# Kernel tuning notes

Hardware: AMD Instinct MI355X
Metric: run time of the kernel (lower is better)

The kernel has to match this reference:

```python
import jax, jax.numpy as jnp
import numpy as np

GROUPS = 4
ITER_N = 5


def conv1x1(x, w, b=None):
    # x: (B,C,N,W), w: (O,C)
    y = jnp.einsum('oc,bcnw->bonw', w, x)
    if b is not None:
        y = y + b[None, :, None, None]
    return y


def instance_norm(x, eps=1e-3):
    mu = x.mean(axis=(2, 3), keepdims=True)
    var = x.var(axis=(2, 3), keepdims=True)
    return (x - mu) * jax.lax.rsqrt(var + eps)


def batch_norm(x, g, b, eps=1e-5):
    mu = x.mean(axis=(0, 2, 3), keepdims=True)
    var = x.var(axis=(0, 2, 3), keepdims=True)
    return (x - mu) * jax.lax.rsqrt(var + eps) * g[None, :, None, None] + b[None, :, None, None]


def group_norm(x, g, b, groups=GROUPS, eps=1e-5):
    B, C, N, W = x.shape
    xg = x.reshape(B, groups, C // groups, N, W)
    mu = xg.mean(axis=(2, 3, 4), keepdims=True)
    var = xg.var(axis=(2, 3, 4), keepdims=True)
    xn = ((xg - mu) * jax.lax.rsqrt(var + eps)).reshape(B, C, N, W)
    return xn * g[None, :, None, None] + b[None, :, None, None]


def ns_sqrtm(A, iterN=ITER_N):
    # A: (..., d, d) SPD. MPNCOV Newton-Schulz matrix square root.
    d = A.shape[-1]
    I = jnp.eye(d, dtype=A.dtype)
    trA = jnp.trace(A, axis1=-2, axis2=-1)[..., None, None]
    An = A / trA
    ZY = 0.5 * (3.0 * I - An)
    Y = An @ ZY
    Z = ZY
    for _ in range(iterN - 2):  # fixed small loop over NS iterations
        ZY = 0.5 * (3.0 * I - Z @ Y)
        Y = Y @ ZY
        Z = ZY @ Z
    ZY = 0.5 * (Y @ (3.0 * I - Z @ Y))
    return ZY * jnp.sqrt(trA)


def covar_attn(feat):
    # feat: (B,C,N,W); per-group covariance pooling + sqrtm + channel reweight
    B, C, N, W = feat.shape
    d = C // GROUPS
    M = N * W
    f = feat.reshape(B, GROUPS, d, M)
    fc = f - f.mean(axis=-1, keepdims=True)
    cov = jnp.einsum('bgim,bgjm->bgij', fc, fc) / M  # == x I_hat x^T
    sq = ns_sqrtm(cov)
    s = sq.mean(axis=-2)  # torch.mean(cov_mat_sqrt, 1): mean over rows -> (B,G,d)
    return s.reshape(B, C, 1, 1) * feat


def setup_inputs() -> dict:
    key = jax.random.key(0)
    ks = jax.random.split(key, 4)
    B, C, N, W = 32, 128, 4000, 1
    scale = 1.0 / np.sqrt(C)
    return {
        'x': jax.random.normal(ks[0], (B, C, N, W), jnp.float32),
        'w_linear': jax.random.normal(ks[1], (C, C), jnp.float32) * scale,
        'gn_gamma': jnp.ones((C,), jnp.float32),
        'gn_beta': jnp.zeros((C,), jnp.float32),
        'bn1_g': jnp.ones((C,), jnp.float32),
        'bn1_b': jnp.zeros((C,), jnp.float32),
        'conv1_w': jax.random.normal(ks[2], (C, C), jnp.float32) * scale,
        'conv1_b': jnp.zeros((C,), jnp.float32),
        'bn2_g': jnp.ones((C,), jnp.float32),
        'bn2_b': jnp.zeros((C,), jnp.float32),
        'conv2_w': jax.random.normal(ks[3], (C, C), jnp.float32) * scale,
        'conv2_b': jnp.zeros((C,), jnp.float32),
    }


def reference(x, w_linear, gn_gamma, gn_beta, bn1_g, bn1_b, conv1_w, conv1_b, bn2_g, bn2_b, conv2_w, conv2_b):
    feat = conv1x1(x, w_linear)
    feat_attn = covar_attn(feat)
    y = group_norm(feat_attn + x, gn_gamma, gn_beta)
    # PointCN residual block (inchannel == outchannel -> identity shortcut)
    h = jax.nn.relu(batch_norm(instance_norm(y), bn1_g, bn1_b))
    h = conv1x1(h, conv1_w, conv1_b)
    h = jax.nn.relu(batch_norm(instance_norm(h), bn2_g, bn2_b))
    h = conv1x1(h, conv2_w, conv2_b)
    return h + y
```

## Files before the change

kernel.cpp:

```cpp
#include <hip/hip_runtime.h>

constexpr int Bn = 32;
constexpr int Cn = 128;
constexpr int Mn = 4000;
constexpr int Gn = 4;
constexpr int Dn = 32;
constexpr float GN_EPS = 1e-5f;
constexpr float IN_EPS = 1e-3f;
constexpr float BN_EPS = 1e-5f;

typedef __attribute__((ext_vector_type(8))) short bf16x8;
typedef __attribute__((ext_vector_type(4))) float f32x4;
typedef __attribute__((ext_vector_type(16))) float f32x16;

__device__ __forceinline__ float bf2f(ushort u) {
    union { unsigned int u; float f; } v;
    v.u = ((unsigned int)u) << 16;
    return v.f;
}
__device__ __forceinline__ ushort f2bf(float f) {
    union { float f; unsigned int u; } v;
    v.f = f;
    unsigned int r = v.u + 0x7FFFu + ((v.u >> 16) & 1u);
    return (ushort)(r >> 16);
}

__global__ void prep_w3(const float* __restrict__ w0, const float* __restrict__ w1,
                        const float* __restrict__ w2, ushort* __restrict__ wb,
                        float* __restrict__ zbase, int zquads) {
    const int i = blockIdx.x * 256 + threadIdx.x;
    const int which = i >> 14;
    const int off = i & 16383;
    const float v = (which == 0) ? w0[off] : (which == 1) ? w1[off] : w2[off];
    wb[i] = f2bf(v);
    if (i < zquads) {
        f32x4 z;
        z[0] = 0.f; z[1] = 0.f; z[2] = 0.f; z[3] = 0.f;
        *(f32x4*)(zbase + (size_t)i * 4) = z;
    }
}

__launch_bounds__(256)
__global__ void prep_xt(const float* __restrict__ x, ushort* __restrict__ xt) {
    __shared__ float tl[128 * 33];
    const int mb = blockIdx.x * 32, b = blockIdx.y;
    const int tid = threadIdx.x;
    const int mi = tid & 31, cg = tid >> 5;
#pragma unroll
    for (int p = 0; p < 16; ++p) {
        const int ci = cg + 8 * p;
        tl[ci * 33 + mi] = x[((size_t)b * Cn + ci) * Mn + mb + mi];
    }
    __syncthreads();
#pragma unroll
    for (int q = 0; q < 2; ++q) {
        const int row = (tid >> 4) + 16 * q;
        const int c8 = (tid & 15) * 8;
        bf16x8 v;
#pragma unroll
        for (int e = 0; e < 8; ++e)
            v[e] = (short)f2bf(tl[(c8 + e) * 33 + row]);
        *(bf16x8*)(xt + ((size_t)b * Mn + mb + row) * Cn + c8) = v;
    }
}

constexpr int WPAD = 136;
constexpr int EP0  = 132;

__launch_bounds__(256, 2)
__global__ void mgemm0_cov(const ushort* __restrict__ Wb,
                           const ushort* __restrict__ src,
                           ushort* __restrict__ dst_bf,
                           float* __restrict__ sf, float* __restrict__ sf2,
                           float* __restrict__ sfxp,
                           float* __restrict__ sxp, float* __restrict__ sx2p,
                           float* __restrict__ covp)
{
    __shared__ ushort Wl[128 * WPAD];
    __shared__ ushort El[64 * EP0];
    const int b = blockIdx.y;
    const int mb0 = blockIdx.x * 256;
    const int tid = threadIdx.x;
    const int wv = tid >> 6, l = tid & 63;
    const int li = l & 15, lg = l >> 4;

#pragma unroll
    for (int p = 0; p < 8; ++p) {
        const int u = tid + 256 * p;
        const int o = u >> 4, c8 = (u & 15) * 8;
        *(bf16x8*)&Wl[o * WPAD + c8] = *(const bf16x8*)(Wb + (size_t)o * 128 + c8);
    }
    __syncthreads();

    f32x16 cacc;
#pragma unroll
    for (int i = 0; i < 16; ++i) cacc[i] = 0.f;
    float s1a[8] = {}, s2a[8] = {}, s3a[8] = {}, s4a[8] = {}, s5a[8] = {};

    const int c8s = (tid & 15) * 8;
    const int cg = wv * 32 + (l & 31);
    const int kb8 = (l >> 5) * 8;

#pragma unroll 1
    for (int t = 0; t < 4; ++t) {
        const int mb = mb0 + t * 64;
        const int ma = mb + wv * 16 + li;
        const bool mok = ma < Mn;
        const size_t qrow = ((size_t)b * Mn + (mok ? ma : (Mn - 1))) * Cn;

        bf16x8 fr[4];
#pragma unroll
        for (int kb = 0; kb < 4; ++kb)
            fr[kb] = *(const bf16x8*)(src + qrow + kb * 32 + 8 * lg);

        f32x4 acc[8];
#pragma unroll
        for (int j = 0; j < 8; ++j)
#pragma unroll
            for (int r = 0; r < 4; ++r) acc[j][r] = 0.f;

#pragma unroll
        for (int kb = 0; kb < 4; ++kb) {
            const int cl = kb * 32 + 8 * lg;
#pragma unroll
            for (int j = 0; j < 8; ++j) {
                const bf16x8 bj = *(const bf16x8*)&Wl[(j * 16 + li) * WPAD + cl];
                acc[j] = __builtin_amdgcn_mfma_f32_16x16x32_bf16(fr[kb], bj, acc[j], 0, 0, 0);
            }
        }

        __syncthreads();
#pragma unroll
        for (int j = 0; j < 8; ++j) {
            const int o = j * 16 + li;
#pragma unroll
            for (int r = 0; r < 4; ++r) {
                const int ml = wv * 16 + lg * 4 + r;
                El[ml * EP0 + o] = (mb + ml < Mn) ? f2bf(acc[j][r]) : (ushort)0;
            }
        }
        __syncthreads();

#pragma unroll
        for (int p = 0; p < 4; ++p) {
            const int row = (tid >> 4) + 16 * p;
            const int m = mb + row;
            const bf16x8 v8 = *(const bf16x8*)&El[row * EP0 + c8s];
            if (m < Mn) {
                const size_t q = ((size_t)b * Mn + m) * Cn + c8s;
                *(bf16x8*)(dst_bf + q) = v8;
                const bf16x8 x8 = *(const bf16x8*)(src + q);
#pragma unroll
                for (int e = 0; e < 8; ++e) {
                    const float f = bf2f((ushort)v8[e]);
                    const float xv = bf2f((ushort)x8[e]);
                    s1a[e] += f;
                    s2a[e] = fmaf(f, f, s2a[e]);
                    s3a[e] = fmaf(f, xv, s3a[e]);
                    s4a[e] += xv;
                    s5a[e] = fmaf(xv, xv, s5a[e]);
                }
            }
        }

#pragma unroll
        for (int ks = 0; ks < 4; ++ks) {
            bf16x8 fgr;
#pragma unroll
            for (int e = 0; e < 8; ++e)
                fgr[e] = (short)El[(ks * 16 + kb8 + e) * EP0 + cg];
            cacc = __builtin_amdgcn_mfma_f32_32x32x16_bf16(fgr, fgr, cacc, 0, 0, 0);
        }
    }

    __syncthreads();
#pragma unroll
    for (int e = 0; e < 8; ++e) {
        s1a[e] += __shfl_xor(s1a[e], 16); s1a[e] += __shfl_xor(s1a[e], 32);
        s2a[e] += __shfl_xor(s2a[e], 16); s2a[e] += __shfl_xor(s2a[e], 32);
        s3a[e] += __shfl_xor(s3a[e], 16); s3a[e] += __shfl_xor(s3a[e], 32);
        s4a[e] += __shfl_xor(s4a[e], 16); s4a[e] += __shfl_xor(s4a[e], 32);
        s5a[e] += __shfl_xor(s5a[e], 16); s5a[e] += __shfl_xor(s5a[e], 32);
    }
    float* red = (float*)El;
    if (l < 16) {
#pragma unroll
        for (int e = 0; e < 8; ++e) {
            red[(wv * 16 + l) * 40 + e]      = s1a[e];
            red[(wv * 16 + l) * 40 + 8 + e]  = s2a[e];
            red[(wv * 16 + l) * 40 + 16 + e] = s3a[e];
            red[(wv * 16 + l) * 40 + 24 + e] = s4a[e];
            red[(wv * 16 + l) * 40 + 32 + e] = s5a[e];
        }
    }
    __syncthreads();
    if (tid < 128) {
        const int oc = tid >> 3, e = tid & 7;
        const int o = oc * 8 + e;
        float t1 = 0.f, t2 = 0.f, t3 = 0.f, t4 = 0.f, t5 = 0.f;
#pragma unroll
        for (int w = 0; w < 4; ++w) {
            t1 += red[(w * 16 + oc) * 40 + e];
            t2 += red[(w * 16 + oc) * 40 + 8 + e];
            t3 += red[(w * 16 + oc) * 40 + 16 + e];
            t4 += red[(w * 16 + oc) * 40 + 24 + e];
            t5 += red[(w * 16 + oc) * 40 + 32 + e];
        }
        atomicAdd(&sf[b * Cn + o], t1);
        atomicAdd(&sf2[b * Cn + o], t2);
        atomicAdd(&sfxp[b * Cn + o], t3);
        atomicAdd(&sxp[b * Cn + o], t4);
        atomicAdd(&sx2p[b * Cn + o], t5);
    }
    float* cvb = covp + (size_t)(b * Gn + wv) * (Dn * Dn);
#pragma unroll
    for (int reg = 0; reg < 16; ++reg) {
        const int i = (reg & 3) + 8 * (reg >> 2) + 4 * (l >> 5);
        const int j = l & 31;
        atomicAdd(&cvb[i * Dn + j], cacc[reg]);
    }
}

constexpr int EPAD = 68;

template <int MODE>
__launch_bounds__(256, 5)
__global__ void mgemm_kernel(const ushort* __restrict__ Wb,
                             const ushort* __restrict__ src,
                             const ushort* __restrict__ xsrc,
                             ushort* __restrict__ dst_bf,
                             float* __restrict__ dst_f32,
                             const float* __restrict__ bias,
                             const float* __restrict__ sarr,
                             const float* __restrict__ tA,
                             const float* __restrict__ tB,
                             const float* __restrict__ Ayc,
                             const float* __restrict__ Byc,
                             const ushort* __restrict__ yfeat,
                             const ushort* __restrict__ yxt,
                             float* __restrict__ sum1,
                             float* __restrict__ sum2)
{
    __shared__ ushort Wl[64 * WPAD];
    __shared__ ushort El[64 * EPAD];
    __shared__ float coefLDS[640];
    const int b = blockIdx.z;
    const int obh = blockIdx.y;
    const int ob = obh * 64;
    const int mb0 = blockIdx.x * 256;
    const int tid = threadIdx.x;
    const int wv = tid >> 6, l = tid & 63;
    const int li = l & 15, lg = l >> 4;

#pragma unroll
    for (int p = 0; p < 4; ++p) {
        const int u = tid + 256 * p;
        const int row = u >> 4, c8 = (u & 15) * 8;
        *(bf16x8*)&Wl[row * WPAD + c8] = *(const bf16x8*)(Wb + (size_t)(ob + row) * 128 + c8);
    }
    {
        const int ncoef = (MODE == 1) ? 384 : 640;
        for (int idx = tid; idx < ncoef; idx += 256) {
            const int arr = idx >> 7, c = idx & 127;
            float v;
            switch (arr) {
                case 0: v = tA[b * Cn + c]; break;
                case 1: v = tB[b * Cn + c]; break;
                case 2: v = sarr[b * Cn + c]; break;
                case 3: v = Ayc[b * Cn + c]; break;
                default: v = Byc[b * Cn + c]; break;
            }
            coefLDS[idx] = v;
        }
    }
    __syncthreads();

    float s1a[8] = {}, s2a[8] = {};
    const int c8l = (tid & 7) * 8;

#pragma unroll 1
    for (int t = 0; t < 4; ++t) {
        const int mb = mb0 + t * 64;
        const int ma = mb + wv * 16 + li;
        const bool mok = ma < Mn;
        const int mc = mok ? ma : (Mn - 1);
        const size_t qrow = ((size_t)b * Mn + mc) * Cn;

        bf16x8 fr[4], xr[4];
#pragma unroll
        for (int kb = 0; kb < 4; ++kb) {
            if (MODE == 1) {
                const int cl = kb * 32 + 8 * lg;
                fr[kb] = *(const bf16x8*)(src + qrow + cl);
                xr[kb] = *(const bf16x8*)(xsrc + qrow + cl);
            } else {
                const size_t q2 = (((size_t)b * 2 + (kb >> 1)) * Mn + mc) * 64 + (kb & 1) * 32 + 8 * lg;
                fr[kb] = *(const bf16x8*)(src + q2);
            }
        }

        f32x4 acc[4];
#pragma unroll
        for (int j = 0; j < 4; ++j)
#pragma unroll
            for (int r = 0; r < 4; ++r) acc[j][r] = 0.f;

#pragma unroll
        for (int kb = 0; kb < 4; ++kb) {
            const int cl = kb * 32 + 8 * lg;
            bf16x8 af;
            if (MODE == 1) {
                const float4 a0 = *(const float4*)&coefLDS[0 + cl];
                const float4 a1 = *(const float4*)&coefLDS[0 + cl + 4];
                const float4 b0 = *(const float4*)&coefLDS[128 + cl];
                const float4 b1 = *(const float4*)&coefLDS[128 + cl + 4];
                const float4 s0 = *(const float4*)&coefLDS[256 + cl];
                const float4 s1 = *(const float4*)&coefLDS[256 + cl + 4];
                const float tAv[8] = {a0.x,a0.y,a0.z,a0.w,a1.x,a1.y,a1.z,a1.w};
                const float tBv[8] = {b0.x,b0.y,b0.z,b0.w,b1.x,b1.y,b1.z,b1.w};
                const float svv[8] = {s0.x,s0.y,s0.z,s0.w,s1.x,s1.y,s1.z,s1.w};
#pragma unroll
                for (int e = 0; e < 8; ++e) {
                    const float vv = fmaf(svv[e], bf2f((ushort)fr[kb][e]), bf2f((ushort)xr[kb][e]));
                    af[e] = (short)f2bf(fmaxf(fmaf(tAv[e], vv, tBv[e]), 0.f));
                }
            } else {
                const float4 a0 = *(const float4*)&coefLDS[0 + cl];
                const float4 a1 = *(const float4*)&coefLDS[0 + cl + 4];
                const float4 b0 = *(const float4*)&coefLDS[128 + cl];
                const float4 b1 = *(const float4*)&coefLDS[128 + cl + 4];
                const float tAv[8] = {a0.x,a0.y,a0.z,a0.w,a1.x,a1.y,a1.z,a1.w};
                const float tBv[8] = {b0.x,b0.y,b0.z,b0.w,b1.x,b1.y,b1.z,b1.w};
#pragma unroll
                for (int e = 0; e < 8; ++e)
                    af[e] = (short)f2bf(fmaxf(fmaf(tAv[e], bf2f((ushort)fr[kb][e]), tBv[e]), 0.f));
            }
#pragma unroll
            for (int j = 0; j < 4; ++j) {
                const bf16x8 bj = *(const bf16x8*)&Wl[(j * 16 + li) * WPAD + cl];
                acc[j] = __builtin_amdgcn_mfma_f32_16x16x32_bf16(af, bj, acc[j], 0, 0, 0);
            }
        }

        if (MODE == 1) {
            __syncthreads();
#pragma unroll
            for (int j = 0; j < 4; ++j) {
                const int o = j * 16 + li;
                const float bv = bias[ob + o];
#pragma unroll
                for (int r = 0; r < 4; ++r) {
                    const int ml = wv * 16 + lg * 4 + r;
                    El[ml * EPAD + o] = f2bf(acc[j][r] + bv);
                }
            }
            __syncthreads();
#pragma unroll
            for (int p = 0; p < 2; ++p) {
                const int row = (tid >> 3) + 32 * p;
                const int m = mb + row;
                const bf16x8 v8 = *(const bf16x8*)&El[row * EPAD + c8l];
                if (m < Mn) {
                    *(bf16x8*)(dst_bf + (((size_t)b * 2 + obh) * Mn + m) * 64 + c8l) = v8;
#pragma unroll
                    for (int e = 0; e < 8; ++e) {
                        const float f = bf2f((ushort)v8[e]);
                        s1a[e] += f;
                        s2a[e] = fmaf(f, f, s2a[e]);
                    }
                }
            }
        } else {
            __syncthreads();
            float* TR = (float*)El;
#pragma unroll
            for (int p = 0; p < 2; ++p) {
                const int row = (tid >> 3) + 32 * p;
                bf16x8 yv;
#pragma unroll
                for (int e = 0; e < 8; ++e) yv[e] = 0;
                if (mb + row < Mn) {
                    const size_t q = ((size_t)b * Mn + mb + row) * Cn + ob + c8l;
                    const bf16x8 f8 = *(const bf16x8*)(yfeat + q);
                    const bf16x8 x8 = *(const bf16x8*)(yxt + q);
#pragma unroll
                    for (int e = 0; e < 8; ++e) {
                        const int c = ob + c8l + e;
                        const float vv = fmaf(coefLDS[256 + c], bf2f((ushort)f8[e]), bf2f((ushort)x8[e]));
                        yv[e] = (short)f2bf(fmaf(coefLDS[384 + c], vv, coefLDS[512 + c]));
                    }
                }
                *(bf16x8*)&El[row * EPAD + c8l] = yv;
            }
            __syncthreads();
#pragma unroll
            for (int j = 0; j < 4; ++j) {
                const int o = j * 16 + li;
                const float bv = bias[ob + o];
#pragma unroll
                for (int r = 0; r < 4; ++r) {
                    const int ml = wv * 16 + lg * 4 + r;
                    acc[j][r] += bv + bf2f(El[ml * EPAD + o]);
                }
            }
#pragma unroll
            for (int h = 0; h < 2; ++h) {
                __syncthreads();
#pragma unroll
                for (int jj = 0; jj < 2; ++jj) {
                    const int j = h * 2 + jj;
#pragma unroll
                    for (int r = 0; r < 4; ++r) {
                        const int ml = wv * 16 + lg * 4 + r;
                        TR[(jj * 16 + li) * EPAD + ml] = acc[j][r];
                    }
                }
                __syncthreads();
#pragma unroll
                for (int p = 0; p < 2; ++p) {
                    const int u = tid + 256 * p;
                    const int ol = u >> 4, q = u & 15;
                    const int m = mb + 4 * q;
                    if (m < Mn) {
                        const f32x4 v = *(const f32x4*)&TR[ol * EPAD + 4 * q];
                        *(f32x4*)(dst_f32 + ((size_t)b * Cn + ob + h * 32 + ol) * Mn + m) = v;
                    }
                }
            }
        }
    }

    if constexpr (MODE == 1) {
#pragma unroll
        for (int e = 0; e < 8; ++e) {
            s1a[e] += __shfl_xor(s1a[e], 8);  s2a[e] += __shfl_xor(s2a[e], 8);
            s1a[e] += __shfl_xor(s1a[e], 16); s2a[e] += __shfl_xor(s2a[e], 16);
            s1a[e] += __shfl_xor(s1a[e], 32); s2a[e] += __shfl_xor(s2a[e], 32);
        }
        __syncthreads();
        float* red = coefLDS;
        if (l < 8) {
#pragma unroll
            for (int e = 0; e < 8; ++e) {
                red[wv * 128 + l * 8 + e] = s1a[e];
                red[wv * 128 + 64 + l * 8 + e] = s2a[e];
            }
        }
        __syncthreads();
        if (tid < 128) {
            const int which = tid >> 6, ol = tid & 63;
            const float v = red[0 * 128 + which * 64 + ol] + red[1 * 128 + which * 64 + ol] +
                            red[2 * 128 + which * 64 + ol] + red[3 * 128 + which * 64 + ol];
            atomicAdd((which ? sum2 : sum1) + b * Cn + ob + ol, v);
        }
    }
}

__device__ __forceinline__ void mm32(float (*A)[33], float (*Bm)[33],
                                     float (*O)[33], int ei, int ej0)
{
    float a0 = 0.f, a1 = 0.f, a2 = 0.f, a3 = 0.f;
#pragma unroll
    for (int k = 0; k < 32; ++k) {
        const float a = A[ei][k];
        a0 = fmaf(a, Bm[k][ej0 + 0], a0);
        a1 = fmaf(a, Bm[k][ej0 + 1], a1);
        a2 = fmaf(a, Bm[k][ej0 + 2], a2);
        a3 = fmaf(a, Bm[k][ej0 + 3], a3);
    }
    O[ei][ej0 + 0] = a0;
    O[ei][ej0 + 1] = a1;
    O[ei][ej0 + 2] = a2;
    O[ei][ej0 + 3] = a3;
    __syncthreads();
}

__launch_bounds__(256)
__global__ void sqrtm_kernel(const float* __restrict__ cov,
                             const float* __restrict__ sf,
                             float* __restrict__ sout)
{
    __shared__ float b0[32][33], b1[32][33], b2[32][33], b3[32][33];
    __shared__ float sh_tr, sh_scale;
    const int bg = blockIdx.x;
    const int b = bg >> 2, g = bg & 3;
    const int tid = threadIdx.x;
    const int ei = (tid * 4) >> 5, ej0 = (tid * 4) & 31;
    const float* cp = cov + (size_t)bg * (Dn * Dn);
    const float* fs = sf + b * Cn + g * Dn;
    const float invM = 1.f / Mn;
    const float mi = fs[ei] * invM;
#pragma unroll
    for (int q = 0; q < 4; ++q)
        b0[ei][ej0 + q] = cp[ei * Dn + ej0 + q] * invM - mi * (fs[ej0 + q] * invM);
    __syncthreads();
    if (tid < 32) {
        float d = b0[tid][tid];
#pragma unroll
        for (int dd = 1; dd < 32; dd <<= 1) d += __shfl_xor(d, dd);
        if (tid == 0) { sh_tr = d; sh_scale = 0.5f * sqrtf(d); }
    }
    __syncthreads();
    const float invtr = 1.f / sh_tr;
#pragma unroll
    for (int q = 0; q < 4; ++q) {
        const float an = b0[ei][ej0 + q] * invtr;
        b0[ei][ej0 + q] = an;
        b1[ei][ej0 + q] = ((ei == ej0 + q) ? 1.5f : 0.f) - 0.5f * an;
    }
    __syncthreads();
    mm32(b0, b1, b2, ei, ej0);
    float (*pY)[33] = b2;
    float (*pZ)[33] = b1;
    float (*pF1)[33] = b0;
    float (*pF2)[33] = b3;
#pragma unroll 1
    for (int it = 0; it < 3; ++it) {
        mm32(pZ, pY, pF1, ei, ej0);
#pragma unroll
        for (int q = 0; q < 4; ++q)
            pF1[ei][ej0 + q] = ((ei == ej0 + q) ? 1.5f : 0.f) - 0.5f * pF1[ei][ej0 + q];
        __syncthreads();
        mm32(pY, pF1, pF2, ei, ej0);
        mm32(pF1, pZ, pY, ei, ej0);
        float (*oldZ)[33] = pZ;
        pZ = pY;
        pY = pF2;
        pF2 = oldZ;
    }
    mm32(pZ, pY, pF1, ei, ej0);
#pragma unroll
    for (int q = 0; q < 4; ++q)
        pF1[ei][ej0 + q] = ((ei == ej0 + q) ? 3.f : 0.f) - pF1[ei][ej0 + q];
    __syncthreads();
    mm32(pY, pF1, pF2, ei, ej0);
    if (tid < 32) {
        float t = 0.f;
#pragma unroll
        for (int i = 0; i < 32; ++i) t += pF2[i][tid];
        sout[b * Cn + g * Dn + tid] = t * sh_scale * (1.f / Dn);
    }
}

__launch_bounds__(1024)
__global__ void coef1_kernel(const float* __restrict__ sf, const float* __restrict__ sf2,
                             const float* __restrict__ sfx, const float* __restrict__ sx,
                             const float* __restrict__ sx2, const float* __restrict__ s,
                             const float* __restrict__ gng, const float* __restrict__ gnb,
                             const float* __restrict__ bn1g, const float* __restrict__ bn1b,
                             float* __restrict__ Ay, float* __restrict__ By,
                             float* __restrict__ Ah, float* __restrict__ Bh)
{
    __shared__ float smv[Bn * Cn];
    __shared__ float sm2[Bn * Cn];
    __shared__ float smu[Bn * Gn], srs[Bn * Gn];
    __shared__ float sV[Cn];
    const int tid = threadIdx.x;
    const float invM = 1.f / Mn;
    for (int p = tid; p < Bn * Cn; p += 1024) {
        const float sv = s[p];
        smv[p] = fmaf(sv, sf[p], sx[p]) * invM;
        sm2[p] = (sv * sv * sf2[p] + 2.f * sv * sfx[p] + sx2[p]) * invM;
    }
    __syncthreads();
    if (tid < Bn * Gn) {
        const int base = tid * Dn;
        float mu = 0.f, e2 = 0.f;
        for (int c = 0; c < Dn; ++c) { mu += smv[base + c]; e2 += sm2[base + c]; }
        mu *= (1.f / Dn); e2 *= (1.f / Dn);
        smu[tid] = mu;
        srs[tid] = rsqrtf(e2 - mu * mu + GN_EPS);
    }
    __syncthreads();
    for (int p = tid; p < Bn * Cn; p += 1024) {
        const int c = p & (Cn - 1);
        const int bg = p >> 5;
        const float ay = srs[bg] * gng[c];
        const float mv = smv[p];
        sm2[p] = ay * ay * (sm2[p] - mv * mv);
    }
    __syncthreads();
    if (tid < Cn) {
        float V = 0.f;
        for (int b = 0; b < Bn; ++b) {
            const float vy = sm2[b * Cn + tid];
            V += vy / (vy + IN_EPS);
        }
        sV[tid] = V * (1.f / Bn);
    }
    __syncthreads();
    for (int p = tid; p < Bn * Cn; p += 1024) {
        const int c = p & (Cn - 1);
        const int bg = p >> 5;
        const float ay = srs[bg] * gng[c];
        const float mv = smv[p];
        const float by = gnb[c] - smu[bg] * ay;
        const float rsin = rsqrtf(sm2[p] + IN_EPS);
        const float ah = ay * rsin * rsqrtf(sV[c] + BN_EPS) * bn1g[c];
        const float bh = bn1b[c] - ah * mv;
        Ay[p] = ay; By[p] = by; Ah[p] = ah; Bh[p] = bh;
    }
}

__launch_bounds__(1024)
__global__ void coef2_kernel(const float* __restrict__ sum1, const float* __restrict__ sum2,
                             const float* __restrict__ bn2g, const float* __restrict__ bn2b,
                             float* __restrict__ A2, float* __restrict__ B2)
{
    __shared__ float svar[Bn * Cn];
    __shared__ float sV[Cn];
    const int tid = threadIdx.x;
    const float invM = 1.f / Mn;
    for (int p = tid; p < Bn * Cn; p += 1024) {
        const float mu = sum1[p] * invM;
        svar[p] = sum2[p] * invM - mu * mu;
    }
    __syncthreads();
    if (tid < Cn) {
        float V = 0.f;
        for (int b = 0; b < Bn; ++b) {
            const float v = svar[b * Cn + tid];
            V += v / (v + IN_EPS);
        }
        sV[tid] = V * (1.f / Bn);
    }
    __syncthreads();
    for (int p = tid; p < Bn * Cn; p += 1024) {
        const int c = p & (Cn - 1);
        const float mu = sum1[p] * invM;
        const float a2 = rsqrtf(svar[p] + IN_EPS) * rsqrtf(sV[c] + BN_EPS) * bn2g[c];
        A2[p] = a2;
        B2[p] = bn2b[c] - a2 * mu;
    }
}

extern "C" void kernel_launch(void* const* d_in, const int* in_sizes, int n_in,
                              void* d_out, int out_size, void* d_ws, size_t ws_size,
                              hipStream_t stream)
{
    const float* x      = (const float*)d_in[0];
    const float* w_lin  = (const float*)d_in[1];
    const float* gn_g   = (const float*)d_in[2];
    const float* gn_b   = (const float*)d_in[3];
    const float* bn1g   = (const float*)d_in[4];
    const float* bn1b   = (const float*)d_in[5];
    const float* conv1w = (const float*)d_in[6];
    const float* conv1b = (const float*)d_in[7];
    const float* bn2g   = (const float*)d_in[8];
    const float* bn2b   = (const float*)d_in[9];
    const float* conv2w = (const float*)d_in[10];
    const float* conv2b = (const float*)d_in[11];
    float* out = (float*)d_out;

    const size_t TS = (size_t)Bn * Mn * Cn;
    ushort* xt    = (ushort*)d_ws;
    ushort* featt = xt + TS;
    ushort* h2t   = featt + TS;
    ushort* wb1   = h2t + TS;
    ushort* wb2   = wb1 + Cn * Cn;
    ushort* wb3   = wb2 + Cn * Cn;
    float*  fbase = (float*)(wb3 + Cn * Cn);
    float* sarr = fbase;
    float* Ay   = sarr + Bn * Cn;
    float* By   = Ay + Bn * Cn;
    float* Ah   = By + Bn * Cn;
    float* Bh   = Ah + Bn * Cn;
    float* A2   = Bh + Bn * Cn;
    float* B2   = A2 + Bn * Cn;
    float* zbase = B2 + Bn * Cn;
    float* cov  = zbase;
    float* sf   = cov + Bn * Gn * Dn * Dn;
    float* sf2  = sf + Bn * Cn;
    float* sfx  = sf2 + Bn * Cn;
    float* sx   = sfx + Bn * Cn;
    float* sx2  = sx + Bn * Cn;
    float* sum1 = sx2 + Bn * Cn;
    float* sum2 = sum1 + Bn * Cn;
    const size_t zfloats = (size_t)Bn * Gn * Dn * Dn + 7 * Bn * Cn;
    const int zquads = (int)(zfloats / 4);

    prep_w3<<<dim3(192), 256, 0, stream>>>(w_lin, conv1w, conv2w, wb1, zbase, zquads);
    prep_xt<<<dim3(Mn / 32, Bn), 256, 0, stream>>>(x, xt);

    mgemm0_cov<<<dim3((Mn + 255) / 256, Bn), 256, 0, stream>>>(
        wb1, xt, featt, sf, sf2, sfx, sx, sx2, cov);

    sqrtm_kernel<<<Bn * Gn, 256, 0, stream>>>(cov, sf, sarr);

    coef1_kernel<<<1, 1024, 0, stream>>>(sf, sf2, sfx, sx, sx2, sarr,
                                         gn_g, gn_b, bn1g, bn1b, Ay, By, Ah, Bh);

    const dim3 ggrid((Mn + 255) / 256, 2, Bn);

    mgemm_kernel<1><<<ggrid, 256, 0, stream>>>(
        wb2, featt, xt, h2t, nullptr, conv1b, sarr, Ah, Bh,
        nullptr, nullptr, nullptr, nullptr, sum1, sum2);

    coef2_kernel<<<1, 1024, 0, stream>>>(sum1, sum2, bn2g, bn2b, A2, B2);

    mgemm_kernel<2><<<ggrid, 256, 0, stream>>>(
        wb3, h2t, nullptr, nullptr, out, conv2b, sarr, A2, B2,
        Ay, By, featt, xt, nullptr, nullptr);
}
```

Baseline: 125.8 us.

## Split first GEMM+covariance kernel over two output-channel halves

The first GEMM/covariance kernel now splits output channels into two 64-wide halves across a new grid dimension. This doubles the block count and lowers per-block LDS so more blocks fit per CU. The feature tensor is stored in a half-split layout, and the downstream GEMM kernels are updated to read that layout. Covariance partials from wave pairs are combined in LDS before the atomics, and the input tile is now read once by each of the two half-blocks.

```diff
diff --git a/kernel.cpp b/kernel.cpp
--- a/kernel.cpp
+++ b/kernel.cpp
@@ -65,9 +65,9 @@
 }
 
 constexpr int WPAD = 136;
-constexpr int EP0  = 132;
-
-__launch_bounds__(256, 2)
+constexpr int EPAD = 68;
+
+__launch_bounds__(256, 4)
 __global__ void mgemm0_cov(const ushort* __restrict__ Wb,
                            const ushort* __restrict__ src,
                            ushort* __restrict__ dst_bf,
@@ -76,19 +76,20 @@
                            float* __restrict__ sxp, float* __restrict__ sx2p,
                            float* __restrict__ covp)
 {
-    __shared__ ushort Wl[128 * WPAD];
-    __shared__ ushort El[64 * EP0];
-    const int b = blockIdx.y;
+    __shared__ ushort Wl[64 * WPAD];
+    __shared__ ushort El[64 * EPAD];
+    const int b = blockIdx.z;
+    const int obh = blockIdx.y, ob = obh * 64;
     const int mb0 = blockIdx.x * 256;
     const int tid = threadIdx.x;
     const int wv = tid >> 6, l = tid & 63;
     const int li = l & 15, lg = l >> 4;
 
 #pragma unroll
-    for (int p = 0; p < 8; ++p) {
+    for (int p = 0; p < 4; ++p) {
         const int u = tid + 256 * p;
-        const int o = u >> 4, c8 = (u & 15) * 8;
-        *(bf16x8*)&Wl[o * WPAD + c8] = *(const bf16x8*)(Wb + (size_t)o * 128 + c8);
+        const int row = u >> 4, c8 = (u & 15) * 8;
+        *(bf16x8*)&Wl[row * WPAD + c8] = *(const bf16x8*)(Wb + (size_t)(ob + row) * 128 + c8);
     }
     __syncthreads();
 
@@ -97,9 +98,10 @@
     for (int i = 0; i < 16; ++i) cacc[i] = 0.f;
     float s1a[8] = {}, s2a[8] = {}, s3a[8] = {}, s4a[8] = {}, s5a[8] = {};
 
-    const int c8s = (tid & 15) * 8;
-    const int cg = wv * 32 + (l & 31);
+    const int c8l = (tid & 7) * 8;
+    const int cg = (wv >> 1) * 32 + (l & 31);
     const int kb8 = (l >> 5) * 8;
+    const int ksbase = 2 * (wv & 1);
 
 #pragma unroll 1
     for (int t = 0; t < 4; ++t) {
@@ -113,9 +115,9 @@
         for (int kb = 0; kb < 4; ++kb)
             fr[kb] = *(const bf16x8*)(src + qrow + kb * 32 + 8 * lg);
 
-        f32x4 acc[8];
-#pragma unroll
-        for (int j = 0; j < 8; ++j)
+        f32x4 acc[4];
+#pragma unroll
+        for (int j = 0; j < 4; ++j)
 #pragma unroll
             for (int r = 0; r < 4; ++r) acc[j][r] = 0.f;
 
@@ -123,7 +125,7 @@
         for (int kb = 0; kb < 4; ++kb) {
             const int cl = kb * 32 + 8 * lg;
 #pragma unroll
-            for (int j = 0; j < 8; ++j) {
+            for (int j = 0; j < 4; ++j) {
                 const bf16x8 bj = *(const bf16x8*)&Wl[(j * 16 + li) * WPAD + cl];
                 acc[j] = __builtin_amdgcn_mfma_f32_16x16x32_bf16(fr[kb], bj, acc[j], 0, 0, 0);
             }
@@ -131,25 +133,24 @@
 
         __syncthreads();
 #pragma unroll
-        for (int j = 0; j < 8; ++j) {
+        for (int j = 0; j < 4; ++j) {
             const int o = j * 16 + li;
 #pragma unroll
             for (int r = 0; r < 4; ++r) {
                 const int ml = wv * 16 + lg * 4 + r;
-                El[ml * EP0 + o] = (mb + ml < Mn) ? f2bf(acc[j][r]) : (ushort)0;
+                El[ml * EPAD + o] = (mb + ml < Mn) ? f2bf(acc[j][r]) : (ushort)0;
             }
         }
         __syncthreads();
 
 #pragma unroll
-        for (int p = 0; p < 4; ++p) {
-            const int row = (tid >> 4) + 16 * p;
+        for (int p = 0; p < 2; ++p) {
+            const int row = (tid >> 3) + 32 * p;
             const int m = mb + row;
-            const bf16x8 v8 = *(const bf16x8*)&El[row * EP0 + c8s];
+            const bf16x8 v8 = *(const bf16x8*)&El[row * EPAD + c8l];
             if (m < Mn) {
-                const size_t q = ((size_t)b * Mn + m) * Cn + c8s;
-                *(bf16x8*)(dst_bf + q) = v8;
-                const bf16x8 x8 = *(const bf16x8*)(src + q);
+                *(bf16x8*)(dst_bf + (((size_t)b * 2 + obh) * Mn + m) * 64 + c8l) = v8;
+                const bf16x8 x8 = *(const bf16x8*)(src + ((size_t)b * Mn + m) * Cn + ob + c8l);
 #pragma unroll
                 for (int e = 0; e < 8; ++e) {
                     const float f = bf2f((ushort)v8[e]);
@@ -164,64 +165,73 @@
         }
 
 #pragma unroll
-        for (int ks = 0; ks < 4; ++ks) {
+        for (int s = 0; s < 2; ++s) {
+            const int ks = ksbase + s;
             bf16x8 fgr;
 #pragma unroll
             for (int e = 0; e < 8; ++e)
-                fgr[e] = (short)El[(ks * 16 + kb8 + e) * EP0 + cg];
+                fgr[e] = (short)El[(ks * 16 + kb8 + e) * EPAD + cg];
             cacc = __builtin_amdgcn_mfma_f32_32x32x16_bf16(fgr, fgr, cacc, 0, 0, 0);
         }
     }
 
     __syncthreads();
+    float* fl = (float*)El;
+    if (wv & 1) {
+#pragma unroll
+        for (int reg = 0; reg < 16; ++reg)
+            fl[(wv >> 1) * 1024 + l * 16 + reg] = cacc[reg];
+    }
+    __syncthreads();
+    if (!(wv & 1)) {
+        float* cvb = covp + ((size_t)b * Gn + obh * 2 + (wv >> 1)) * (Dn * Dn);
+#pragma unroll
+        for (int reg = 0; reg < 16; ++reg) {
+            const int i = (reg & 3) + 8 * (reg >> 2) + 4 * (l >> 5);
+            const int j = l & 31;
+            atomicAdd(&cvb[i * Dn + j], cacc[reg] + fl[(wv >> 1) * 1024 + l * 16 + reg]);
+        }
+    }
+    __syncthreads();
+
 #pragma unroll
     for (int e = 0; e < 8; ++e) {
-        s1a[e] += __shfl_xor(s1a[e], 16); s1a[e] += __shfl_xor(s1a[e], 32);
-        s2a[e] += __shfl_xor(s2a[e], 16); s2a[e] += __shfl_xor(s2a[e], 32);
-        s3a[e] += __shfl_xor(s3a[e], 16); s3a[e] += __shfl_xor(s3a[e], 32);
-        s4a[e] += __shfl_xor(s4a[e], 16); s4a[e] += __shfl_xor(s4a[e], 32);
-        s5a[e] += __shfl_xor(s5a[e], 16); s5a[e] += __shfl_xor(s5a[e], 32);
-    }
-    float* red = (float*)El;
-    if (l < 16) {
+        s1a[e] += __shfl_xor(s1a[e], 8);  s1a[e] += __shfl_xor(s1a[e], 16); s1a[e] += __shfl_xor(s1a[e], 32);
+        s2a[e] += __shfl_xor(s2a[e], 8);  s2a[e] += __shfl_xor(s2a[e], 16); s2a[e] += __shfl_xor(s2a[e], 32);
+        s3a[e] += __shfl_xor(s3a[e], 8);  s3a[e] += __shfl_xor(s3a[e], 16); s3a[e] += __shfl_xor(s3a[e], 32);
+        s4a[e] += __shfl_xor(s4a[e], 8);  s4a[e] += __shfl_xor(s4a[e], 16); s4a[e] += __shfl_xor(s4a[e], 32);
+        s5a[e] += __shfl_xor(s5a[e], 8);  s5a[e] += __shfl_xor(s5a[e], 16); s5a[e] += __shfl_xor(s5a[e], 32);
+    }
+    if (l < 8) {
 #pragma unroll
         for (int e = 0; e < 8; ++e) {
-            red[(wv * 16 + l) * 40 + e]      = s1a[e];
-            red[(wv * 16 + l) * 40 + 8 + e]  = s2a[e];
-            red[(wv * 16 + l) * 40 + 16 + e] = s3a[e];
-            red[(wv * 16 + l) * 40 + 24 + e] = s4a[e];
-            red[(wv * 16 + l) * 40 + 32 + e] = s5a[e];
-        }
-    }
-    __syncthreads();
-    if (tid < 128) {
-        const int oc = tid >> 3, e = tid & 7;
-        const int o = oc * 8 + e;
+            fl[wv * 320 + l * 40 + e]      = s1a[e];
+            fl[wv * 320 + l * 40 + 8 + e]  = s2a[e];
+            fl[wv * 320 + l * 40 + 16 + e] = s3a[e];
+            fl[wv * 320 + l * 40 + 24 + e] = s4a[e];
+            fl[wv * 320 + l * 40 + 32 + e] = s5a[e];
+        }
+    }
+    __syncthreads();
+    if (tid < 64) {
+        const int lg8 = tid >> 3, e = tid & 7;
         float t1 = 0.f, t2 = 0.f, t3 = 0.f, t4 = 0.f, t5 = 0.f;
 #pragma unroll
         for (int w = 0; w < 4; ++w) {
-            t1 += red[(w * 16 + oc) * 40 + e];
-            t2 += red[(w * 16 + oc) * 40 + 8 + e];
-            t3 += red[(w * 16 + oc) * 40 + 16 + e];
-            t4 += red[(w * 16 + oc) * 40 + 24 + e];
-            t5 += red[(w * 16 + oc) * 40 + 32 + e];
-        }
-        atomicAdd(&sf[b * Cn + o], t1);
-        atomicAdd(&sf2[b * Cn + o], t2);
-        atomicAdd(&sfxp[b * Cn + o], t3);
-        atomicAdd(&sxp[b * Cn + o], t4);
-        atomicAdd(&sx2p[b * Cn + o], t5);
-    }
-    float* cvb = covp + (size_t)(b * Gn + wv) * (Dn * Dn);
-#pragma unroll
-    for (int reg = 0; reg < 16; ++reg) {
-        const int i = (reg & 3) + 8 * (reg >> 2) + 4 * (l >> 5);
-        const int j = l & 31;
-        atomicAdd(&cvb[i * Dn + j], cacc[reg]);
-    }
-}
-
-constexpr int EPAD = 68;
+            t1 += fl[w * 320 + lg8 * 40 + e];
+            t2 += fl[w * 320 + lg8 * 40 + 8 + e];
+            t3 += fl[w * 320 + lg8 * 40 + 16 + e];
+            t4 += fl[w * 320 + lg8 * 40 + 24 + e];
+            t5 += fl[w * 320 + lg8 * 40 + 32 + e];
+        }
+        const int c = b * Cn + ob + tid;
+        atomicAdd(&sf[c], t1);
+        atomicAdd(&sf2[c], t2);
+        atomicAdd(&sfxp[c], t3);
+        atomicAdd(&sxp[c], t4);
+        atomicAdd(&sx2p[c], t5);
+    }
+}
 
 template <int MODE>
 __launch_bounds__(256, 5)
@@ -289,14 +299,10 @@
         bf16x8 fr[4], xr[4];
 #pragma unroll
         for (int kb = 0; kb < 4; ++kb) {
-            if (MODE == 1) {
-                const int cl = kb * 32 + 8 * lg;
-                fr[kb] = *(const bf16x8*)(src + qrow + cl);
-                xr[kb] = *(const bf16x8*)(xsrc + qrow + cl);
-            } else {
-                const size_t q2 = (((size_t)b * 2 + (kb >> 1)) * Mn + mc) * 64 + (kb & 1) * 32 + 8 * lg;
-                fr[kb] = *(const bf16x8*)(src + q2);
-            }
+            const size_t q2 = (((size_t)b * 2 + (kb >> 1)) * Mn + mc) * 64 + (kb & 1) * 32 + 8 * lg;
+            fr[kb] = *(const bf16x8*)(src + q2);
+            if (MODE == 1)
+                xr[kb] = *(const bf16x8*)(xsrc + qrow + kb * 32 + 8 * lg);
         }
 
         f32x4 acc[4];
@@ -380,9 +386,10 @@
 #pragma unroll
                 for (int e = 0; e < 8; ++e) yv[e] = 0;
                 if (mb + row < Mn) {
-                    const size_t q = ((size_t)b * Mn + mb + row) * Cn + ob + c8l;
-                    const bf16x8 f8 = *(const bf16x8*)(yfeat + q);
-                    const bf16x8 x8 = *(const bf16x8*)(yxt + q);
+                    const size_t qf = (((size_t)b * 2 + obh) * Mn + mb + row) * 64 + c8l;
+                    const size_t qx = ((size_t)b * Mn + mb + row) * Cn + ob + c8l;
+                    const bf16x8 f8 = *(const bf16x8*)(yfeat + qf);
+                    const bf16x8 x8 = *(const bf16x8*)(yxt + qx);
 #pragma unroll
                     for (int e = 0; e < 8; ++e) {
                         const int c = ob + c8l + e;
@@ -682,7 +689,7 @@
     prep_w3<<<dim3(192), 256, 0, stream>>>(w_lin, conv1w, conv2w, wb1, zbase, zquads);
     prep_xt<<<dim3(Mn / 32, Bn), 256, 0, stream>>>(x, xt);
 
-    mgemm0_cov<<<dim3((Mn + 255) / 256, Bn), 256, 0, stream>>>(
+    mgemm0_cov<<<dim3((Mn + 255) / 256, 2, Bn), 256, 0, stream>>>(
         wb1, xt, featt, sf, sf2, sfx, sx, sx2, cov);
 
     sqrtm_kernel<<<Bn * Gn, 256, 0, stream>>>(cov, sf, sarr);
```

New measurement: 126.1 us. No clear change (+0.2%).
